# Performance work log

Measured on AMD Instinct MI355X. Metric: run time of the kernel, lower is better.

The kernel has to match this reference:

```python
import jax, jax.numpy as jnp
import numpy as np

EPS = 1e-5

def setup_inputs() -> dict:
    key = jax.random.key(0)
    ks = jax.random.split(key, 8)
    B, Cin, H, W = 16, 64, 512, 64
    Cout = 128  # out_channels == mid_channels (default) == NL1D channels
    return {
        "x": jax.random.normal(ks[0], (B, Cin, H, W), dtype=jnp.float32),
        "conv_w": jax.random.normal(ks[1], (Cout, Cin, 3, 3), dtype=jnp.float32) * 0.05,
        "bn1_g": jnp.ones((Cout,), jnp.float32),
        "bn1_b": jnp.zeros((Cout,), jnp.float32),
        "g_w": jax.random.normal(ks[2], (Cout, Cout), dtype=jnp.float32) * 0.05,
        "g_b": jnp.zeros((Cout,), jnp.float32),
        "out_w": jax.random.normal(ks[3], (Cout, Cout), dtype=jnp.float32) * 0.05,
        "out_b": jnp.zeros((Cout,), jnp.float32),
        "bn2_g": jnp.ones((Cout,), jnp.float32),
        "bn2_b": jnp.zeros((Cout,), jnp.float32),
    }

def _bn_train(x, gamma, beta):
    # BatchNorm2d in training mode: batch stats over (B, H, W) per channel
    mu = jnp.mean(x, axis=(0, 2, 3), keepdims=True)
    var = jnp.mean(jnp.square(x - mu), axis=(0, 2, 3), keepdims=True)
    xn = (x - mu) * jax.lax.rsqrt(var + EPS)
    return xn * gamma[None, :, None, None] + beta[None, :, None, None]

def reference(x, conv_w, bn1_g, bn1_b, g_w, g_b, out_w, out_b, bn2_g, bn2_b):
    # conv: 3x3, reflect padding, no bias -> BN -> ReLU
    xp = jnp.pad(x, ((0, 0), (0, 0), (1, 1), (1, 1)), mode="reflect")
    h = jax.lax.conv_general_dilated(
        xp, conv_w, window_strides=(1, 1), padding="VALID",
        dimension_numbers=("NCHW", "OIHW", "NCHW"))
    h = jax.nn.relu(_bn_train(h, bn1_g, bn1_b))  # [B, C, H, W]

    # NL1D
    B, C, Hh, W = h.shape
    xm = jnp.mean(h, axis=3)  # [B, C, H]
    # layer_norm over (C, H) per batch element, no affine
    mu = jnp.mean(xm, axis=(1, 2), keepdims=True)
    var = jnp.mean(jnp.square(xm - mu), axis=(1, 2), keepdims=True)
    xn = (xm - mu) * jax.lax.rsqrt(var + EPS)

    f = jnp.einsum("bch,bck->bhk", xn, xn) / jnp.sqrt(jnp.float32(C))
    f = jax.nn.softmax(f, axis=2)  # [B, H, H]

    y = jnp.einsum("mc,bch->bmh", g_w, xn) + g_b[None, :, None]  # conv1d 1x1
    y = jnp.einsum("bhk,bmk->bmh", f, y)  # bmm(f, y^T)^T
    y = jnp.einsum("om,bmh->boh", out_w, y) + out_b[None, :, None]  # [B, C, H]

    out = h + y[:, :, :, None]  # broadcast == repeat over W
    return jax.nn.silu(_bn_train(out, bn2_g, bn2_b))
```

## Files before the change

### kernel.cpp

```cpp
#include <hip/hip_runtime.h>
#include <stdint.h>

typedef __attribute__((ext_vector_type(8))) short short8;
typedef __attribute__((ext_vector_type(4))) float f32x4;

typedef const __attribute__((address_space(1))) unsigned int* gas_u32p;
typedef __attribute__((address_space(3))) unsigned int* las_u32p;

__device__ __forceinline__ unsigned short f2bf(float f){
  union{float f; unsigned u;} v; v.f = f;
  unsigned r = v.u + 0x7FFFu + ((v.u >> 16) & 1u);
  return (unsigned short)(r >> 16);
}
__device__ __forceinline__ void dec8(uint4 d, float* r){
  union{unsigned a; float f;} t;
  t.a = (d.x & 0xFFFFu) << 16; r[0]=t.f; t.a = d.x & 0xFFFF0000u; r[1]=t.f;
  t.a = (d.y & 0xFFFFu) << 16; r[2]=t.f; t.a = d.y & 0xFFFF0000u; r[3]=t.f;
  t.a = (d.z & 0xFFFFu) << 16; r[4]=t.f; t.a = d.z & 0xFFFF0000u; r[5]=t.f;
  t.a = (d.w & 0xFFFFu) << 16; r[6]=t.f; t.a = d.w & 0xFFFF0000u; r[7]=t.f;
}

__global__ __launch_bounds__(256) void k_prep(const float* __restrict__ cw,
                                              unsigned short* __restrict__ wA){
  int i = blockIdx.x*256 + threadIdx.x;
  if(i >= 18*128*32) return;
  int kk = i & 31, m = (i >> 5) & 127, ks = i >> 12;
  int k = ks*32 + kk;
  int pos = k >> 6, cin = k & 63;
  int dh = pos/3, dw = pos - dh*3;
  wA[i] = f2bf(cw[((m*64 + cin)*3 + dh)*3 + dw]);
}

__global__ __launch_bounds__(256) void k_xbf(const float* __restrict__ x,
                                             unsigned short* __restrict__ xbf){
  const int h = blockIdx.x, b = blockIdx.y;
  __shared__ float L[64][65];
  const int t = threadIdx.x;
  #pragma unroll
  for(int i=0;i<4;++i){
    int idx = i*256 + t;
    int c = idx >> 4, w0 = (idx & 15) * 4;
    const float* p = x + (((size_t)b*64 + c)*512 + h)*64 + w0;
    float4 v = *(const float4*)p;
    L[c][w0] = v.x; L[c][w0+1] = v.y; L[c][w0+2] = v.z; L[c][w0+3] = v.w;
  }
  __syncthreads();
  unsigned short* dst = xbf + (((size_t)b*512 + h) << 12);
  #pragma unroll
  for(int i=0;i<8;++i){
    int idx = i*256 + t;
    int w = idx >> 5, c2 = (idx & 31)*2;
    unsigned pk = (unsigned)f2bf(L[c2][w]) | ((unsigned)f2bf(L[c2+1][w]) << 16);
    *(unsigned*)(dst + (w<<6) + c2) = pk;
  }
}

__global__ __launch_bounds__(256, 2) void k_conv(
    const unsigned short* __restrict__ xbf, const unsigned short* __restrict__ wA,
    unsigned short* __restrict__ craw, float* __restrict__ sum_slots,
    float* __restrict__ sq_slots)
{
  const int b = blockIdx.y;
  const int bx = blockIdx.x;
  const int hx = (bx & 7)*16 + (bx >> 3);
  const int h0 = hx * 4;
  __shared__ __align__(16) unsigned short xs[6*4096];
  __shared__ float red[2][128];
  const int t = threadIdx.x;
  const int lane = t & 63, wv = t >> 6;
  for(int r = wv; r < 6; r += 4){
    int hin = h0 - 1 + r;
    hin = hin < 0 ? 1 : (hin > 511 ? 510 : hin);
    const unsigned short* rsrc = xbf + (((size_t)b*512 + hin) << 12);
    unsigned short* ldsrow = &xs[r*4096];
    #pragma unroll
    for(int it=0; it<8; ++it){
      int o = it*1024 + lane*16;
      int w = o >> 7;
      int q = o & 127;
      int so = (w << 7) + (q ^ (((w >> 1) & 7) << 4));
      __builtin_amdgcn_global_load_lds(
          (gas_u32p)(const void*)((const char*)rsrc + so),
          (las_u32p)(void*)(ldsrow + it*512), 16, 0, 0);
    }
  }
  const int r15 = lane & 15, quad = lane >> 4;
  int P[4][3];
  #pragma unroll
  for(int nt=0;nt<4;++nt){
    int wn = (nt>>1)*32 + 2*r15 + (nt&1);
    #pragma unroll
    for(int dw=0;dw<3;++dw){
      int wi = wn + dw - 1;
      wi = wi < 0 ? 1 : (wi > 63 ? 62 : wi);
      int s = ((wi >> 1) & 7) << 4;
      P[nt][dw] = (wi << 7) + ((quad*16) ^ (s & 0x30)) + (s & 0x40);
    }
  }
  f32x4 acc[8][4];
  #pragma unroll
  for(int mt=0;mt<8;++mt)
    #pragma unroll
    for(int nt=0;nt<4;++nt){ f32x4 z = {0.f,0.f,0.f,0.f}; acc[mt][nt] = z; }
  const unsigned short* wbase = wA + r15*32 + quad*8;
  __syncthreads();
  const char* xsb = (const char*)xs;
  #pragma unroll
  for(int ks=0; ks<18; ++ks){
    const int pos = ks >> 1;
    const int dh = pos/3, dw = pos - dh*3;
    const int kbit = (ks & 1) << 6;
    const int rowoff = (wv + dh)*8192;
    short8 a[8];
    const unsigned short* wk = wbase + ks*4096;
    #pragma unroll
    for(int mt=0;mt<8;++mt) a[mt] = *(const short8*)(wk + mt*512);
    short8 bfr[4];
    #pragma unroll
    for(int nt=0;nt<4;++nt)
      bfr[nt] = *(const short8*)(xsb + rowoff + (P[nt][dw] ^ kbit));
    #pragma unroll
    for(int mt=0;mt<8;++mt){
      #pragma unroll
      for(int nt=0;nt<4;++nt)
        acc[mt][nt] = __builtin_amdgcn_mfma_f32_16x16x32_bf16(a[mt], bfr[nt], acc[mt][nt], 0,0,0);
    }
  }
  {
    size_t obase = (((size_t)b*128)*512 + (size_t)(h0+wv))*64 + 2*r15;
    #pragma unroll
    for(int mt=0;mt<8;++mt){
      #pragma unroll
      for(int rg=0;rg<4;++rg){
        int co = mt*16 + quad*4 + rg;
        unsigned pk0 = (unsigned)f2bf(acc[mt][0][rg]) | ((unsigned)f2bf(acc[mt][1][rg]) << 16);
        unsigned pk1 = (unsigned)f2bf(acc[mt][2][rg]) | ((unsigned)f2bf(acc[mt][3][rg]) << 16);
        *(unsigned*)(craw + obase + (size_t)co*32768) = pk0;
        *(unsigned*)(craw + obase + (size_t)co*32768 + 32) = pk1;
      }
    }
  }
  if(t < 128){ red[0][t] = 0.f; red[1][t] = 0.f; }
  __syncthreads();
  #pragma unroll
  for(int mt=0;mt<8;++mt){
    #pragma unroll
    for(int rg=0;rg<4;++rg){
      float s = acc[mt][0][rg] + acc[mt][1][rg] + acc[mt][2][rg] + acc[mt][3][rg];
      float q = acc[mt][0][rg]*acc[mt][0][rg] + acc[mt][1][rg]*acc[mt][1][rg]
              + acc[mt][2][rg]*acc[mt][2][rg] + acc[mt][3][rg]*acc[mt][3][rg];
      #pragma unroll
      for(int m=1;m<16;m<<=1){ s += __shfl_xor(s, m); q += __shfl_xor(q, m); }
      if(r15 == 0){
        int co = mt*16 + quad*4 + rg;
        atomicAdd(&red[0][co], s);
        atomicAdd(&red[1][co], q);
      }
    }
  }
  __syncthreads();
  if(t < 128){
    int slot = bx & 63;
    atomicAdd(&sum_slots[t*64 + slot], red[0][t]);
    atomicAdd(&sq_slots[t*64 + slot], red[1][t]);
  }
}

__global__ __launch_bounds__(256) void k_bn1fin(
    const float* __restrict__ sum_slots, const float* __restrict__ sq_slots,
    const float* __restrict__ g1, const float* __restrict__ b1,
    float* __restrict__ s1, float* __restrict__ t1)
{
  int c = threadIdx.x; if(c >= 128) return;
  double S = 0.0, Q = 0.0;
  for(int s=0;s<64;++s){ S += (double)sum_slots[c*64+s]; Q += (double)sq_slots[c*64+s]; }
  const double N = 524288.0;
  double mu = S/N, var = Q/N - mu*mu;
  float sc = (float)((double)g1[c] / sqrt(var + 1e-5));
  s1[c] = sc;
  t1[c] = (float)((double)b1[c] - mu*(double)sc);
}

__global__ __launch_bounds__(256) void k_passB(
    const unsigned short* __restrict__ craw, const float* __restrict__ s1,
    const float* __restrict__ t1, float* __restrict__ xm,
    float* __restrict__ Sh, float* __restrict__ Qh,
    float* __restrict__ lnS, float* __restrict__ lnQ)
{
  const int c = blockIdx.x, b = blockIdx.y;
  const int t = threadIdx.x, wv = t >> 6, l = t & 63;
  const float sc = s1[c], sf = t1[c];
  const unsigned short* base = craw + (((size_t)b*128 + c)*512)*64;
  float* xrow = xm + ((size_t)b*128 + c)*512;
  float sa = 0.f, qa = 0.f, la = 0.f;
  for(int it=0; it<16; ++it){
    int row = it*32 + wv*8 + (l >> 3);
    int w0 = (l & 7)*8;
    uint4 d = *(const uint4*)(base + (size_t)row*64 + w0);
    float r[8]; dec8(d, r);
    float tot = 0.f;
    #pragma unroll
    for(int j=0;j<8;++j){
      float v = sc*r[j] + sf;
      v = v > 0.f ? v : 0.f;
      tot += v; sa += v; qa += v*v;
    }
    tot += __shfl_xor(tot, 1); tot += __shfl_xor(tot, 2); tot += __shfl_xor(tot, 4);
    if((l & 7) == 0){
      float mv = tot * (1.f/64.f);
      xrow[row] = mv;
      la += mv*mv;
    }
  }
  #pragma unroll
  for(int m=1;m<64;m<<=1){
    sa += __shfl_xor(sa, m); qa += __shfl_xor(qa, m); la += __shfl_xor(la, m);
  }
  __shared__ float rs[4], rq[4], rl[4];
  if(l == 0){ rs[wv]=sa; rq[wv]=qa; rl[wv]=la; }
  __syncthreads();
  if(t == 0){
    float S = rs[0]+rs[1]+rs[2]+rs[3];
    float Q = rq[0]+rq[1]+rq[2]+rq[3];
    float L = rl[0]+rl[1]+rl[2]+rl[3];
    atomicAdd(&Sh[c], S);
    atomicAdd(&Qh[c], Q);
    atomicAdd(&lnS[b], S * (1.f/64.f));
    atomicAdd(&lnQ[b], L);
  }
}

__global__ __launch_bounds__(256) void k_lnfin(
    const float* __restrict__ lnS, const float* __restrict__ lnQ,
    float* __restrict__ ln_mu, float* __restrict__ ln_rs)
{
  int b = threadIdx.x; if(b >= 16) return;
  double mu = (double)lnS[b] / 65536.0;
  double var = (double)lnQ[b] / 65536.0 - mu*mu;
  ln_mu[b] = (float)mu;
  ln_rs[b] = (float)(1.0 / sqrt(var + 1e-5));
}

__global__ __launch_bounds__(256) void k_f(const float* __restrict__ xm,
    const float* __restrict__ ln_mu, const float* __restrict__ ln_rs,
    float* __restrict__ f)
{
  const int kt = blockIdx.x, ht = blockIdx.y, b = blockIdx.z;
  __shared__ __align__(16) float Xh[128][64];
  __shared__ __align__(16) float Xk[128][64];
  const int t = threadIdx.x;
  const int h0 = ht*64, k0 = kt*64;
  const float mu = ln_mu[b], rs = ln_rs[b];
  for(int i=0;i<32;++i){
    int idx = t + i*256;
    int c = idx >> 6, hh = idx & 63;
    const float* src = xm + ((size_t)b*128 + c)*512;
    Xh[c][hh] = (src[h0 + hh] - mu) * rs;
    Xk[c][hh] = (src[k0 + hh] - mu) * rs;
  }
  __syncthreads();
  const int tx = t & 15, ty = t >> 4;
  float acc[4][4] = {{0}};
  for(int c=0;c<128;++c){
    f32x4 a = *(const f32x4*)&Xh[c][ty*4];
    f32x4 bb = *(const f32x4*)&Xk[c][tx*4];
    #pragma unroll
    for(int i=0;i<4;++i)
      #pragma unroll
      for(int j=0;j<4;++j) acc[i][j] += a[i]*bb[j];
  }
  const float s = 0.088388347648318447f;
  #pragma unroll
  for(int i=0;i<4;++i){
    f32x4 o;
    o[0]=acc[i][0]*s; o[1]=acc[i][1]*s; o[2]=acc[i][2]*s; o[3]=acc[i][3]*s;
    *(f32x4*)&f[((size_t)b*512 + h0 + ty*4 + i)*512 + k0 + tx*4] = o;
  }
}

__global__ __launch_bounds__(256) void k_sm(float* __restrict__ f)
{
  const int bid = blockIdx.x;
  const int b = bid >> 7, h4 = bid & 127;
  const int t = threadIdx.x, wv = t >> 6, l = t & 63;
  float* row = f + ((size_t)b*512 + h4*4 + wv)*512;
  f32x4 v0 = *(const f32x4*)&row[l*8];
  f32x4 v1 = *(const f32x4*)&row[l*8 + 4];
  float mx = v0[0];
  #pragma unroll
  for(int j=1;j<4;++j) mx = fmaxf(mx, v0[j]);
  #pragma unroll
  for(int j=0;j<4;++j) mx = fmaxf(mx, v1[j]);
  #pragma unroll
  for(int m=1;m<64;m<<=1) mx = fmaxf(mx, __shfl_xor(mx, m));
  float sum = 0.f;
  #pragma unroll
  for(int j=0;j<4;++j){ v0[j] = __expf(v0[j]-mx); sum += v0[j]; }
  #pragma unroll
  for(int j=0;j<4;++j){ v1[j] = __expf(v1[j]-mx); sum += v1[j]; }
  #pragma unroll
  for(int m=1;m<64;m<<=1) sum += __shfl_xor(sum, m);
  float inv = 1.f / sum;
  #pragma unroll
  for(int j=0;j<4;++j){ v0[j] *= inv; v1[j] *= inv; }
  *(f32x4*)&row[l*8] = v0;
  *(f32x4*)&row[l*8+4] = v1;
}

__global__ __launch_bounds__(256) void k_y1(
    const float* __restrict__ xm, const float* __restrict__ ln_mu,
    const float* __restrict__ ln_rs, const float* __restrict__ gw,
    const float* __restrict__ gb, float* __restrict__ y1)
{
  const int kt = blockIdx.x, b = blockIdx.y;
  __shared__ __align__(16) float GT[128][128];
  __shared__ __align__(16) float XN[128][68];
  const int t = threadIdx.x;
  const int k0 = kt*64;
  const float mu = ln_mu[b], rs = ln_rs[b];
  for(int i=0;i<64;++i){
    int idx = t + i*256;
    int o = idx & 127, c = idx >> 7;
    GT[c][o] = gw[o*128 + c];
  }
  for(int i=0;i<32;++i){
    int idx = t + i*256;
    int c = idx >> 6, kk = idx & 63;
    XN[c][kk] = (xm[((size_t)b*128 + c)*512 + k0 + kk] - mu) * rs;
  }
  __syncthreads();
  const int tx = t & 15, ty = t >> 4;
  float acc[8][4] = {{0}};
  for(int c=0;c<128;++c){
    f32x4 a0 = *(const f32x4*)&GT[c][ty*8];
    f32x4 a1 = *(const f32x4*)&GT[c][ty*8+4];
    f32x4 bv = *(const f32x4*)&XN[c][tx*4];
    #pragma unroll
    for(int j=0;j<4;++j){
      #pragma unroll
      for(int i=0;i<4;++i){ acc[i][j] += a0[i]*bv[j]; acc[i+4][j] += a1[i]*bv[j]; }
    }
  }
  #pragma unroll
  for(int i=0;i<8;++i){
    int m = ty*8 + i;
    float bias = gb[m];
    f32x4 o;
    #pragma unroll
    for(int j=0;j<4;++j) o[j] = acc[i][j] + bias;
    *(f32x4*)&y1[((size_t)b*128 + m)*512 + k0 + tx*4] = o;
  }
}

__global__ __launch_bounds__(256) void k_y2(
    const float* __restrict__ f, const float* __restrict__ y1,
    float* __restrict__ y2t)
{
  const int ht = blockIdx.x, b = blockIdx.y;
  __shared__ __align__(16) float FT[64][36];
  __shared__ __align__(16) float Y1T[64][132];
  const int t = threadIdx.x;
  const int h0 = ht*32;
  const int tx = t & 15, ty = t >> 4;
  float acc[2][8] = {{0}};
  for(int kc=0;kc<8;++kc){
    int k0 = kc*64;
    __syncthreads();
    for(int i=0;i<8;++i){
      int idx = t + i*256;
      int k = idx & 63, hh = idx >> 6;
      FT[k][hh] = f[((size_t)b*512 + h0 + hh)*512 + k0 + k];
    }
    for(int i=0;i<32;++i){
      int idx = t + i*256;
      int k = idx & 63, m = idx >> 6;
      Y1T[k][m] = y1[((size_t)b*128 + m)*512 + k0 + k];
    }
    __syncthreads();
    for(int kk=0;kk<64;++kk){
      float a0 = FT[kk][ty*2], a1 = FT[kk][ty*2+1];
      f32x4 b0 = *(const f32x4*)&Y1T[kk][tx*8];
      f32x4 b1 = *(const f32x4*)&Y1T[kk][tx*8+4];
      #pragma unroll
      for(int j=0;j<4;++j){
        acc[0][j]   += a0*b0[j]; acc[1][j]   += a1*b0[j];
        acc[0][j+4] += a0*b1[j]; acc[1][j+4] += a1*b1[j];
      }
    }
  }
  #pragma unroll
  for(int i=0;i<2;++i){
    int h = h0 + ty*2 + i;
    f32x4 o0, o1;
    #pragma unroll
    for(int j=0;j<4;++j){ o0[j]=acc[i][j]; o1[j]=acc[i][j+4]; }
    float* dst = y2t + ((size_t)b*512 + h)*128 + tx*8;
    *(f32x4*)dst = o0;
    *(f32x4*)(dst+4) = o1;
  }
}

__global__ __launch_bounds__(256) void k_y3(
    const float* __restrict__ y2t, const float* __restrict__ ow,
    const float* __restrict__ obv, float* __restrict__ y3)
{
  const int ht = blockIdx.x, b = blockIdx.y;
  __shared__ __align__(16) float WT[128][128];
  __shared__ __align__(16) float Y2[128][36];
  const int t = threadIdx.x;
  const int h0 = ht*32;
  for(int i=0;i<64;++i){
    int idx = t + i*256;
    int o = idx & 127, m = idx >> 7;
    WT[m][o] = ow[o*128 + m];
  }
  for(int i=0;i<16;++i){
    int idx = t + i*256;
    int m = idx & 127, hh = idx >> 7;
    Y2[m][hh] = y2t[((size_t)b*512 + h0 + hh)*128 + m];
  }
  __syncthreads();
  const int tx = t & 15, ty = t >> 4;
  float acc[8][2] = {{0}};
  for(int m=0;m<128;++m){
    f32x4 a0 = *(const f32x4*)&WT[m][ty*8];
    f32x4 a1 = *(const f32x4*)&WT[m][ty*8+4];
    float b0 = Y2[m][tx*2], b1 = Y2[m][tx*2+1];
    #pragma unroll
    for(int i=0;i<4;++i){
      acc[i][0]   += a0[i]*b0; acc[i][1]   += a0[i]*b1;
      acc[i+4][0] += a1[i]*b0; acc[i+4][1] += a1[i]*b1;
    }
  }
  #pragma unroll
  for(int i=0;i<8;++i){
    int o = ty*8 + i;
    float bias = obv[o];
    float2 v; v.x = acc[i][0] + bias; v.y = acc[i][1] + bias;
    *(float2*)&y3[((size_t)b*128 + o)*512 + h0 + tx*2] = v;
  }
}

__global__ __launch_bounds__(256) void k_ystats(
    const float* __restrict__ y3, const float* __restrict__ xm,
    float* __restrict__ Sy, float* __restrict__ Syy, float* __restrict__ Sxy)
{
  const int c = blockIdx.x;
  const int t = threadIdx.x, wv = t >> 6, l = t & 63;
  float s=0.f, ss=0.f, sx=0.f;
  for(int i=0;i<32;++i){
    int idx = t + i*256;
    int b = idx >> 9, h = idx & 511;
    size_t off = ((size_t)b*128 + c)*512 + h;
    float v = y3[off], u = xm[off];
    s += v; ss += v*v; sx += v*u;
  }
  #pragma unroll
  for(int m=1;m<64;m<<=1){ s += __shfl_xor(s,m); ss += __shfl_xor(ss,m); sx += __shfl_xor(sx,m); }
  __shared__ float r1[4], r2[4], r3[4];
  if(l == 0){ r1[wv]=s; r2[wv]=ss; r3[wv]=sx; }
  __syncthreads();
  if(t == 0){
    Sy[c]  = r1[0]+r1[1]+r1[2]+r1[3];
    Syy[c] = r2[0]+r2[1]+r2[2]+r2[3];
    Sxy[c] = r3[0]+r3[1]+r3[2]+r3[3];
  }
}

__global__ __launch_bounds__(256) void k_bn2fin(
    const float* __restrict__ Sh, const float* __restrict__ Qh,
    const float* __restrict__ Sy, const float* __restrict__ Syy,
    const float* __restrict__ Sxy, const float* __restrict__ g2,
    const float* __restrict__ b2, float* __restrict__ s2, float* __restrict__ t2)
{
  int c = threadIdx.x; if(c >= 128) return;
  const double N = 524288.0;
  double S2 = (double)Sh[c] + 64.0*(double)Sy[c];
  double Q2 = (double)Qh[c] + 128.0*(double)Sxy[c] + 64.0*(double)Syy[c];
  double mu = S2/N, var = Q2/N - mu*mu;
  float sc = (float)((double)g2[c] / sqrt(var + 1e-5));
  s2[c] = sc;
  t2[c] = (float)((double)b2[c] - mu*(double)sc);
}

__global__ __launch_bounds__(256) void k_final(
    const unsigned short* __restrict__ craw, const float* __restrict__ s1,
    const float* __restrict__ t1, const float* __restrict__ y3,
    const float* __restrict__ s2, const float* __restrict__ t2,
    float* __restrict__ out)
{
  const int c = blockIdx.x, b = blockIdx.y;
  const int t = threadIdx.x, wv = t >> 6, l = t & 63;
  const float a1 = s1[c], c1 = t1[c], a2 = s2[c], c2 = t2[c];
  const size_t rb = ((size_t)b*128 + c)*512;
  const unsigned short* base = craw + rb*64;
  const float* yrow = y3 + rb;
  float* ob = out + rb*64;
  for(int it=0; it<16; ++it){
    int row = it*32 + wv*8 + (l >> 3);
    int w0 = (l & 7)*8;
    uint4 d = *(const uint4*)(base + (size_t)row*64 + w0);
    float yv = yrow[row];
    float r[8]; dec8(d, r);
    f32x4 o0, o1;
    #pragma unroll
    for(int j=0;j<8;++j){
      float h = a1*r[j] + c1; h = h > 0.f ? h : 0.f;
      float z = a2*(h + yv) + c2;
      float val = z * __builtin_amdgcn_rcpf(1.f + __expf(-z));
      if(j < 4) o0[j] = val; else o1[j-4] = val;
    }
    *(f32x4*)(ob + (size_t)row*64 + w0) = o0;
    *(f32x4*)(ob + (size_t)row*64 + w0 + 4) = o1;
  }
}

extern "C" void kernel_launch(void* const* d_in, const int* in_sizes, int n_in,
                              void* d_out, int out_size, void* d_ws, size_t ws_size,
                              hipStream_t stream)
{
  const float* x      = (const float*)d_in[0];
  const float* conv_w = (const float*)d_in[1];
  const float* bn1_g  = (const float*)d_in[2];
  const float* bn1_b  = (const float*)d_in[3];
  const float* g_w    = (const float*)d_in[4];
  const float* g_b    = (const float*)d_in[5];
  const float* out_w  = (const float*)d_in[6];
  const float* out_b  = (const float*)d_in[7];
  const float* bn2_g  = (const float*)d_in[8];
  const float* bn2_b  = (const float*)d_in[9];
  float* out = (float*)d_out;
  char* ws = (char*)d_ws;

  float* sum_slots = (float*)(ws);
  float* sq_slots  = (float*)(ws + 32768);
  float* Sh        = (float*)(ws + 65536);
  float* Qh        = (float*)(ws + 66048);
  float* lnS       = (float*)(ws + 66560);
  float* lnQ       = (float*)(ws + 66624);
  float* s1        = (float*)(ws + 66688);
  float* t1        = (float*)(ws + 67200);
  float* ln_mu     = (float*)(ws + 67712);
  float* ln_rs     = (float*)(ws + 67776);
  float* Sy        = (float*)(ws + 67840);
  float* Syy       = (float*)(ws + 68352);
  float* Sxy       = (float*)(ws + 68864);
  float* s2        = (float*)(ws + 69376);
  float* t2        = (float*)(ws + 69888);
  unsigned short* wA = (unsigned short*)(ws + 70400);
  float* y3        = (float*)(ws + 217856);
  unsigned short* craw = (unsigned short*)(ws + 4412160);

  float* xm  = out;
  float* y1  = out + 2*(1u<<20);
  float* y2t = out + 3*(1u<<20);
  float* f   = out + 4*(1u<<20);
  unsigned short* xbf = (unsigned short*)((char*)out + (size_t)64*1024*1024);

  hipMemsetAsync(ws, 0, 66688, stream);
  hipLaunchKernelGGL(k_prep,   dim3(288),      dim3(256), 0, stream, conv_w, wA);
  hipLaunchKernelGGL(k_xbf,    dim3(512,16),   dim3(256), 0, stream, x, xbf);
  hipLaunchKernelGGL(k_conv,   dim3(128,16),   dim3(256), 0, stream, xbf, wA, craw, sum_slots, sq_slots);
  hipLaunchKernelGGL(k_bn1fin, dim3(1),        dim3(128), 0, stream, sum_slots, sq_slots, bn1_g, bn1_b, s1, t1);
  hipLaunchKernelGGL(k_passB,  dim3(128,16),   dim3(256), 0, stream, craw, s1, t1, xm, Sh, Qh, lnS, lnQ);
  hipLaunchKernelGGL(k_lnfin,  dim3(1),        dim3(64),  0, stream, lnS, lnQ, ln_mu, ln_rs);
  hipLaunchKernelGGL(k_f,      dim3(8,8,16),   dim3(256), 0, stream, xm, ln_mu, ln_rs, f);
  hipLaunchKernelGGL(k_sm,     dim3(2048),     dim3(256), 0, stream, f);
  hipLaunchKernelGGL(k_y1,     dim3(8,16),     dim3(256), 0, stream, xm, ln_mu, ln_rs, g_w, g_b, y1);
  hipLaunchKernelGGL(k_y2,     dim3(16,16),    dim3(256), 0, stream, f, y1, y2t);
  hipLaunchKernelGGL(k_y3,     dim3(16,16),    dim3(256), 0, stream, y2t, out_w, out_b, y3);
  hipLaunchKernelGGL(k_ystats, dim3(128),      dim3(256), 0, stream, y3, xm, Sy, Syy, Sxy);
  hipLaunchKernelGGL(k_bn2fin, dim3(1),        dim3(128), 0, stream, Sh, Qh, Sy, Syy, Sxy, bn2_g, bn2_b, s2, t2);
  hipLaunchKernelGGL(k_final,  dim3(128,16),   dim3(256), 0, stream, craw, s1, t1, y3, s2, t2, out);
}
```

Measured before the change: 798.5 us.

## Fuse attention scores, softmax, matmuls and y-stats into one kernel

Replaces k_f, k_sm, k_y2, k_y3 and k_ystats with a single k_att kernel. Each block computes a 32-row slice of scores, applies softmax, multiplies by y1, applies out_w, and accumulates BN2 statistics into slotted atomics, all in shared memory. This removes the 16MB f matrix round trip and several launches. It also vectorises the k_y1 loads and makes the conv output stores nontemporal. The cost is a large shared-memory footprint (about 118KB per block) and only 256 blocks, which limits occupancy.

```diff
diff --git a/kernel.cpp b/kernel.cpp
--- a/kernel.cpp
+++ b/kernel.cpp
@@ -135,8 +135,8 @@
         int co = mt*16 + quad*4 + rg;
         unsigned pk0 = (unsigned)f2bf(acc[mt][0][rg]) | ((unsigned)f2bf(acc[mt][1][rg]) << 16);
         unsigned pk1 = (unsigned)f2bf(acc[mt][2][rg]) | ((unsigned)f2bf(acc[mt][3][rg]) << 16);
-        *(unsigned*)(craw + obase + (size_t)co*32768) = pk0;
-        *(unsigned*)(craw + obase + (size_t)co*32768 + 32) = pk1;
+        __builtin_nontemporal_store(pk0, (unsigned*)(craw + obase + (size_t)co*32768));
+        __builtin_nontemporal_store(pk1, (unsigned*)(craw + obase + (size_t)co*32768 + 32));
       }
     }
   }
@@ -241,100 +241,40 @@
   ln_rs[b] = (float)(1.0 / sqrt(var + 1e-5));
 }
 
-__global__ __launch_bounds__(256) void k_f(const float* __restrict__ xm,
-    const float* __restrict__ ln_mu, const float* __restrict__ ln_rs,
-    float* __restrict__ f)
-{
-  const int kt = blockIdx.x, ht = blockIdx.y, b = blockIdx.z;
-  __shared__ __align__(16) float Xh[128][64];
-  __shared__ __align__(16) float Xk[128][64];
-  const int t = threadIdx.x;
-  const int h0 = ht*64, k0 = kt*64;
-  const float mu = ln_mu[b], rs = ln_rs[b];
-  for(int i=0;i<32;++i){
-    int idx = t + i*256;
-    int c = idx >> 6, hh = idx & 63;
-    const float* src = xm + ((size_t)b*128 + c)*512;
-    Xh[c][hh] = (src[h0 + hh] - mu) * rs;
-    Xk[c][hh] = (src[k0 + hh] - mu) * rs;
-  }
-  __syncthreads();
-  const int tx = t & 15, ty = t >> 4;
-  float acc[4][4] = {{0}};
-  for(int c=0;c<128;++c){
-    f32x4 a = *(const f32x4*)&Xh[c][ty*4];
-    f32x4 bb = *(const f32x4*)&Xk[c][tx*4];
-    #pragma unroll
-    for(int i=0;i<4;++i)
-      #pragma unroll
-      for(int j=0;j<4;++j) acc[i][j] += a[i]*bb[j];
-  }
-  const float s = 0.088388347648318447f;
-  #pragma unroll
-  for(int i=0;i<4;++i){
-    f32x4 o;
-    o[0]=acc[i][0]*s; o[1]=acc[i][1]*s; o[2]=acc[i][2]*s; o[3]=acc[i][3]*s;
-    *(f32x4*)&f[((size_t)b*512 + h0 + ty*4 + i)*512 + k0 + tx*4] = o;
-  }
-}
-
-__global__ __launch_bounds__(256) void k_sm(float* __restrict__ f)
-{
-  const int bid = blockIdx.x;
-  const int b = bid >> 7, h4 = bid & 127;
-  const int t = threadIdx.x, wv = t >> 6, l = t & 63;
-  float* row = f + ((size_t)b*512 + h4*4 + wv)*512;
-  f32x4 v0 = *(const f32x4*)&row[l*8];
-  f32x4 v1 = *(const f32x4*)&row[l*8 + 4];
-  float mx = v0[0];
-  #pragma unroll
-  for(int j=1;j<4;++j) mx = fmaxf(mx, v0[j]);
-  #pragma unroll
-  for(int j=0;j<4;++j) mx = fmaxf(mx, v1[j]);
-  #pragma unroll
-  for(int m=1;m<64;m<<=1) mx = fmaxf(mx, __shfl_xor(mx, m));
-  float sum = 0.f;
-  #pragma unroll
-  for(int j=0;j<4;++j){ v0[j] = __expf(v0[j]-mx); sum += v0[j]; }
-  #pragma unroll
-  for(int j=0;j<4;++j){ v1[j] = __expf(v1[j]-mx); sum += v1[j]; }
-  #pragma unroll
-  for(int m=1;m<64;m<<=1) sum += __shfl_xor(sum, m);
-  float inv = 1.f / sum;
-  #pragma unroll
-  for(int j=0;j<4;++j){ v0[j] *= inv; v1[j] *= inv; }
-  *(f32x4*)&row[l*8] = v0;
-  *(f32x4*)&row[l*8+4] = v1;
-}
-
 __global__ __launch_bounds__(256) void k_y1(
     const float* __restrict__ xm, const float* __restrict__ ln_mu,
     const float* __restrict__ ln_rs, const float* __restrict__ gw,
     const float* __restrict__ gb, float* __restrict__ y1)
 {
   const int kt = blockIdx.x, b = blockIdx.y;
-  __shared__ __align__(16) float GT[128][128];
-  __shared__ __align__(16) float XN[128][68];
+  __shared__ __align__(16) float GT[128*132];
+  __shared__ __align__(16) float XN[128*68];
   const int t = threadIdx.x;
   const int k0 = kt*64;
   const float mu = ln_mu[b], rs = ln_rs[b];
-  for(int i=0;i<64;++i){
+  #pragma unroll
+  for(int i=0;i<16;++i){
     int idx = t + i*256;
-    int o = idx & 127, c = idx >> 7;
-    GT[c][o] = gw[o*128 + c];
-  }
-  for(int i=0;i<32;++i){
+    int c4 = (idx & 31)*4, o = idx >> 5;
+    float4 v = *(const float4*)&gw[o*128 + c4];
+    GT[(c4+0)*132 + o] = v.x; GT[(c4+1)*132 + o] = v.y;
+    GT[(c4+2)*132 + o] = v.z; GT[(c4+3)*132 + o] = v.w;
+  }
+  #pragma unroll
+  for(int i=0;i<8;++i){
     int idx = t + i*256;
-    int c = idx >> 6, kk = idx & 63;
-    XN[c][kk] = (xm[((size_t)b*128 + c)*512 + k0 + kk] - mu) * rs;
+    int kk4 = (idx & 15)*4, c = idx >> 4;
+    float4 v = *(const float4*)&xm[((size_t)b*128 + c)*512 + k0 + kk4];
+    XN[c*68 + kk4 + 0] = (v.x - mu)*rs; XN[c*68 + kk4 + 1] = (v.y - mu)*rs;
+    XN[c*68 + kk4 + 2] = (v.z - mu)*rs; XN[c*68 + kk4 + 3] = (v.w - mu)*rs;
   }
   __syncthreads();
   const int tx = t & 15, ty = t >> 4;
   float acc[8][4] = {{0}};
   for(int c=0;c<128;++c){
-    f32x4 a0 = *(const f32x4*)&GT[c][ty*8];
-    f32x4 a1 = *(const f32x4*)&GT[c][ty*8+4];
-    f32x4 bv = *(const f32x4*)&XN[c][tx*4];
+    f32x4 a0 = *(const f32x4*)&GT[c*132 + ty*8];
+    f32x4 a1 = *(const f32x4*)&GT[c*132 + ty*8 + 4];
+    f32x4 bv = *(const f32x4*)&XN[c*68 + tx*4];
     #pragma unroll
     for(int j=0;j<4;++j){
       #pragma unroll
@@ -352,131 +292,182 @@
   }
 }
 
-__global__ __launch_bounds__(256) void k_y2(
-    const float* __restrict__ f, const float* __restrict__ y1,
-    float* __restrict__ y2t)
+__global__ __launch_bounds__(256) void k_att(
+    const float* __restrict__ xm, const float* __restrict__ ln_mu,
+    const float* __restrict__ ln_rs, const float* __restrict__ y1,
+    const float* __restrict__ ow, const float* __restrict__ obv,
+    float* __restrict__ y3,
+    float* __restrict__ SyS, float* __restrict__ SyyS, float* __restrict__ SxyS)
 {
   const int ht = blockIdx.x, b = blockIdx.y;
-  __shared__ __align__(16) float FT[64][36];
-  __shared__ __align__(16) float Y1T[64][132];
+  const int h0 = ht*32;
+  const int SP = 528;
+  __shared__ __align__(16) float S[32*528];
+  __shared__ __align__(16) float XH[128*32];
+  __shared__ __align__(16) float BUF[8704];
   const int t = threadIdx.x;
-  const int h0 = ht*32;
   const int tx = t & 15, ty = t >> 4;
-  float acc[2][8] = {{0}};
-  for(int kc=0;kc<8;++kc){
-    int k0 = kc*64;
-    __syncthreads();
+  const int lane = t & 63, wv = t >> 6;
+  const float mu = ln_mu[b], rs = ln_rs[b];
+  const float* xb = xm + (size_t)b*128*512;
+  #pragma unroll
+  for(int i=0;i<4;++i){
+    int idx = t + i*256;
+    int hh4 = (idx & 7)*4, c = idx >> 3;
+    float4 v = *(const float4*)&xb[(size_t)c*512 + h0 + hh4];
+    XH[c*32 + hh4 + 0] = (v.x - mu)*rs; XH[c*32 + hh4 + 1] = (v.y - mu)*rs;
+    XH[c*32 + hh4 + 2] = (v.z - mu)*rs; XH[c*32 + hh4 + 3] = (v.w - mu)*rs;
+  }
+  const float sscale = 0.088388347648318447f;
+  for(int kt=0;kt<8;++kt){
+    int k0 = kt*64;
+    #pragma unroll
     for(int i=0;i<8;++i){
       int idx = t + i*256;
-      int k = idx & 63, hh = idx >> 6;
-      FT[k][hh] = f[((size_t)b*512 + h0 + hh)*512 + k0 + k];
-    }
-    for(int i=0;i<32;++i){
+      int kk4 = (idx & 15)*4, c = idx >> 4;
+      float4 v = *(const float4*)&xb[(size_t)c*512 + k0 + kk4];
+      BUF[c*68 + kk4 + 0] = (v.x - mu)*rs; BUF[c*68 + kk4 + 1] = (v.y - mu)*rs;
+      BUF[c*68 + kk4 + 2] = (v.z - mu)*rs; BUF[c*68 + kk4 + 3] = (v.w - mu)*rs;
+    }
+    __syncthreads();
+    float acc[2][4] = {{0}};
+    for(int c=0;c<128;++c){
+      float a0 = XH[c*32 + ty*2];
+      float a1 = XH[c*32 + ty*2 + 1];
+      f32x4 bv = *(const f32x4*)&BUF[c*68 + tx*4];
+      #pragma unroll
+      for(int j=0;j<4;++j){ acc[0][j] += a0*bv[j]; acc[1][j] += a1*bv[j]; }
+    }
+    #pragma unroll
+    for(int i=0;i<2;++i){
+      f32x4 o;
+      #pragma unroll
+      for(int j=0;j<4;++j) o[j] = acc[i][j]*sscale;
+      *(f32x4*)&S[(ty*2+i)*SP + k0 + tx*4] = o;
+    }
+    __syncthreads();
+  }
+  #pragma unroll
+  for(int rr=0;rr<8;++rr){
+    int row = wv*8 + rr;
+    float* rowp = &S[row*SP];
+    f32x4 v0 = *(const f32x4*)&rowp[lane*8];
+    f32x4 v1 = *(const f32x4*)&rowp[lane*8 + 4];
+    float mx = v0[0];
+    #pragma unroll
+    for(int j=1;j<4;++j) mx = fmaxf(mx, v0[j]);
+    #pragma unroll
+    for(int j=0;j<4;++j) mx = fmaxf(mx, v1[j]);
+    #pragma unroll
+    for(int m=1;m<64;m<<=1) mx = fmaxf(mx, __shfl_xor(mx, m));
+    float sum = 0.f;
+    #pragma unroll
+    for(int j=0;j<4;++j){ v0[j] = __expf(v0[j]-mx); sum += v0[j]; }
+    #pragma unroll
+    for(int j=0;j<4;++j){ v1[j] = __expf(v1[j]-mx); sum += v1[j]; }
+    #pragma unroll
+    for(int m=1;m<64;m<<=1) sum += __shfl_xor(sum, m);
+    float inv = 1.f / sum;
+    #pragma unroll
+    for(int j=0;j<4;++j){ v0[j] *= inv; v1[j] *= inv; }
+    *(f32x4*)&rowp[lane*8] = v0;
+    *(f32x4*)&rowp[lane*8+4] = v1;
+  }
+  __syncthreads();
+  float y2a[2][8] = {{0}};
+  for(int kt=0;kt<8;++kt){
+    int k0 = kt*64;
+    #pragma unroll
+    for(int i=0;i<8;++i){
       int idx = t + i*256;
-      int k = idx & 63, m = idx >> 6;
-      Y1T[k][m] = y1[((size_t)b*128 + m)*512 + k0 + k];
+      int kk4 = (idx & 15)*4, m = idx >> 4;
+      float4 v = *(const float4*)&y1[((size_t)b*128 + m)*512 + k0 + kk4];
+      BUF[(kk4+0)*132 + m] = v.x; BUF[(kk4+1)*132 + m] = v.y;
+      BUF[(kk4+2)*132 + m] = v.z; BUF[(kk4+3)*132 + m] = v.w;
     }
     __syncthreads();
     for(int kk=0;kk<64;++kk){
-      float a0 = FT[kk][ty*2], a1 = FT[kk][ty*2+1];
-      f32x4 b0 = *(const f32x4*)&Y1T[kk][tx*8];
-      f32x4 b1 = *(const f32x4*)&Y1T[kk][tx*8+4];
+      float a0 = S[(ty*2)*SP + k0 + kk];
+      float a1 = S[(ty*2+1)*SP + k0 + kk];
+      f32x4 b0 = *(const f32x4*)&BUF[kk*132 + tx*8];
+      f32x4 b1 = *(const f32x4*)&BUF[kk*132 + tx*8 + 4];
       #pragma unroll
       for(int j=0;j<4;++j){
-        acc[0][j]   += a0*b0[j]; acc[1][j]   += a1*b0[j];
-        acc[0][j+4] += a0*b1[j]; acc[1][j+4] += a1*b1[j];
+        y2a[0][j]   += a0*b0[j]; y2a[1][j]   += a1*b0[j];
+        y2a[0][j+4] += a0*b1[j]; y2a[1][j+4] += a1*b1[j];
       }
     }
-  }
-  #pragma unroll
-  for(int i=0;i<2;++i){
-    int h = h0 + ty*2 + i;
-    f32x4 o0, o1;
-    #pragma unroll
-    for(int j=0;j<4;++j){ o0[j]=acc[i][j]; o1[j]=acc[i][j+4]; }
-    float* dst = y2t + ((size_t)b*512 + h)*128 + tx*8;
-    *(f32x4*)dst = o0;
-    *(f32x4*)(dst+4) = o1;
-  }
-}
-
-__global__ __launch_bounds__(256) void k_y3(
-    const float* __restrict__ y2t, const float* __restrict__ ow,
-    const float* __restrict__ obv, float* __restrict__ y3)
-{
-  const int ht = blockIdx.x, b = blockIdx.y;
-  __shared__ __align__(16) float WT[128][128];
-  __shared__ __align__(16) float Y2[128][36];
-  const int t = threadIdx.x;
-  const int h0 = ht*32;
-  for(int i=0;i<64;++i){
-    int idx = t + i*256;
-    int o = idx & 127, m = idx >> 7;
-    WT[m][o] = ow[o*128 + m];
-  }
+    __syncthreads();
+  }
+  #pragma unroll
+  for(int i=0;i<2;++i)
+    #pragma unroll
+    for(int j=0;j<8;++j)
+      BUF[(ty*2+i)*131 + tx*8 + j] = y2a[i][j];
+  float* OWT = S;
+  #pragma unroll
   for(int i=0;i<16;++i){
     int idx = t + i*256;
-    int m = idx & 127, hh = idx >> 7;
-    Y2[m][hh] = y2t[((size_t)b*512 + h0 + hh)*128 + m];
-  }
-  __syncthreads();
-  const int tx = t & 15, ty = t >> 4;
-  float acc[8][2] = {{0}};
+    int m4 = (idx & 31)*4, o = idx >> 5;
+    float4 v = *(const float4*)&ow[o*128 + m4];
+    OWT[(m4+0)*132 + o] = v.x; OWT[(m4+1)*132 + o] = v.y;
+    OWT[(m4+2)*132 + o] = v.z; OWT[(m4+3)*132 + o] = v.w;
+  }
+  __syncthreads();
+  float a2[2][8] = {{0}};
   for(int m=0;m<128;++m){
-    f32x4 a0 = *(const f32x4*)&WT[m][ty*8];
-    f32x4 a1 = *(const f32x4*)&WT[m][ty*8+4];
-    float b0 = Y2[m][tx*2], b1 = Y2[m][tx*2+1];
-    #pragma unroll
-    for(int i=0;i<4;++i){
-      acc[i][0]   += a0[i]*b0; acc[i][1]   += a0[i]*b1;
-      acc[i+4][0] += a1[i]*b0; acc[i+4][1] += a1[i]*b1;
-    }
-  }
-  #pragma unroll
-  for(int i=0;i<8;++i){
-    int o = ty*8 + i;
+    f32x4 w0 = *(const f32x4*)&OWT[m*132 + ty*8];
+    f32x4 w1 = *(const f32x4*)&OWT[m*132 + ty*8 + 4];
+    float h0v = BUF[(tx*2)*131 + m];
+    float h1v = BUF[(tx*2+1)*131 + m];
+    #pragma unroll
+    for(int j=0;j<4;++j){
+      a2[0][j]   += w0[j]*h0v; a2[1][j]   += w0[j]*h1v;
+      a2[0][j+4] += w1[j]*h0v; a2[1][j+4] += w1[j]*h1v;
+    }
+  }
+  const int slot = ((ht<<4) | b) & 31;
+  #pragma unroll
+  for(int j=0;j<8;++j){
+    int o = ty*8 + j;
     float bias = obv[o];
-    float2 v; v.x = acc[i][0] + bias; v.y = acc[i][1] + bias;
-    *(float2*)&y3[((size_t)b*128 + o)*512 + h0 + tx*2] = v;
-  }
-}
-
-__global__ __launch_bounds__(256) void k_ystats(
-    const float* __restrict__ y3, const float* __restrict__ xm,
-    float* __restrict__ Sy, float* __restrict__ Syy, float* __restrict__ Sxy)
-{
-  const int c = blockIdx.x;
-  const int t = threadIdx.x, wv = t >> 6, l = t & 63;
-  float s=0.f, ss=0.f, sx=0.f;
-  for(int i=0;i<32;++i){
-    int idx = t + i*256;
-    int b = idx >> 9, h = idx & 511;
-    size_t off = ((size_t)b*128 + c)*512 + h;
-    float v = y3[off], u = xm[off];
-    s += v; ss += v*v; sx += v*u;
-  }
-  #pragma unroll
-  for(int m=1;m<64;m<<=1){ s += __shfl_xor(s,m); ss += __shfl_xor(ss,m); sx += __shfl_xor(sx,m); }
-  __shared__ float r1[4], r2[4], r3[4];
-  if(l == 0){ r1[wv]=s; r2[wv]=ss; r3[wv]=sx; }
-  __syncthreads();
-  if(t == 0){
-    Sy[c]  = r1[0]+r1[1]+r1[2]+r1[3];
-    Syy[c] = r2[0]+r2[1]+r2[2]+r2[3];
-    Sxy[c] = r3[0]+r3[1]+r3[2]+r3[3];
+    float v0 = a2[0][j] + bias;
+    float v1 = a2[1][j] + bias;
+    size_t off = ((size_t)b*128 + o)*512 + h0 + tx*2;
+    float2 st; st.x = v0; st.y = v1;
+    *(float2*)&y3[off] = st;
+    float2 xv = *(const float2*)&xm[off];
+    float sy_ = v0 + v1;
+    float syy_ = v0*v0 + v1*v1;
+    float sxy_ = v0*xv.x + v1*xv.y;
+    #pragma unroll
+    for(int m=1;m<16;m<<=1){
+      sy_ += __shfl_xor(sy_, m); syy_ += __shfl_xor(syy_, m); sxy_ += __shfl_xor(sxy_, m);
+    }
+    if(tx == 0){
+      atomicAdd(&SyS[o*32 + slot], sy_);
+      atomicAdd(&SyyS[o*32 + slot], syy_);
+      atomicAdd(&SxyS[o*32 + slot], sxy_);
+    }
   }
 }
 
 __global__ __launch_bounds__(256) void k_bn2fin(
     const float* __restrict__ Sh, const float* __restrict__ Qh,
-    const float* __restrict__ Sy, const float* __restrict__ Syy,
-    const float* __restrict__ Sxy, const float* __restrict__ g2,
+    const float* __restrict__ SyS, const float* __restrict__ SyyS,
+    const float* __restrict__ SxyS, const float* __restrict__ g2,
     const float* __restrict__ b2, float* __restrict__ s2, float* __restrict__ t2)
 {
   int c = threadIdx.x; if(c >= 128) return;
+  double Sy = 0.0, Syy = 0.0, Sxy = 0.0;
+  for(int s=0;s<32;++s){
+    Sy  += (double)SyS[c*32+s];
+    Syy += (double)SyyS[c*32+s];
+    Sxy += (double)SxyS[c*32+s];
+  }
   const double N = 524288.0;
-  double S2 = (double)Sh[c] + 64.0*(double)Sy[c];
-  double Q2 = (double)Qh[c] + 128.0*(double)Sxy[c] + 64.0*(double)Syy[c];
+  double S2 = (double)Sh[c] + 64.0*Sy;
+  double Q2 = (double)Qh[c] + 128.0*Sxy + 64.0*Syy;
   double mu = S2/N, var = Q2/N - mu*mu;
   float sc = (float)((double)g2[c] / sqrt(var + 1e-5));
   s2[c] = sc;
@@ -534,6 +525,9 @@
 
   float* sum_slots = (float*)(ws);
   float* sq_slots  = (float*)(ws + 32768);
+  float* SyS       = (float*)(ws);
+  float* SyyS      = (float*)(ws + 16384);
+  float* SxyS      = (float*)(ws + 32768);
   float* Sh        = (float*)(ws + 65536);
   float* Qh        = (float*)(ws + 66048);
   float* lnS       = (float*)(ws + 66560);
@@ -542,19 +536,14 @@
   float* t1        = (float*)(ws + 67200);
   float* ln_mu     = (float*)(ws + 67712);
   float* ln_rs     = (float*)(ws + 67776);
-  float* Sy        = (float*)(ws + 67840);
-  float* Syy       = (float*)(ws + 68352);
-  float* Sxy       = (float*)(ws + 68864);
-  float* s2        = (float*)(ws + 69376);
-  float* t2        = (float*)(ws + 69888);
+  float* s2        = (float*)(ws + 67840);
+  float* t2        = (float*)(ws + 68352);
   unsigned short* wA = (unsigned short*)(ws + 70400);
   float* y3        = (float*)(ws + 217856);
   unsigned short* craw = (unsigned short*)(ws + 4412160);
 
   float* xm  = out;
   float* y1  = out + 2*(1u<<20);
-  float* y2t = out + 3*(1u<<20);
-  float* f   = out + 4*(1u<<20);
   unsigned short* xbf = (unsigned short*)((char*)out + (size_t)64*1024*1024);
 
   hipMemsetAsync(ws, 0, 66688, stream);
@@ -562,14 +551,11 @@
   hipLaunchKernelGGL(k_xbf,    dim3(512,16),   dim3(256), 0, stream, x, xbf);
   hipLaunchKernelGGL(k_conv,   dim3(128,16),   dim3(256), 0, stream, xbf, wA, craw, sum_slots, sq_slots);
   hipLaunchKernelGGL(k_bn1fin, dim3(1),        dim3(128), 0, stream, sum_slots, sq_slots, bn1_g, bn1_b, s1, t1);
+  hipMemsetAsync(ws, 0, 49152, stream);
   hipLaunchKernelGGL(k_passB,  dim3(128,16),   dim3(256), 0, stream, craw, s1, t1, xm, Sh, Qh, lnS, lnQ);
   hipLaunchKernelGGL(k_lnfin,  dim3(1),        dim3(64),  0, stream, lnS, lnQ, ln_mu, ln_rs);
-  hipLaunchKernelGGL(k_f,      dim3(8,8,16),   dim3(256), 0, stream, xm, ln_mu, ln_rs, f);
-  hipLaunchKernelGGL(k_sm,     dim3(2048),     dim3(256), 0, stream, f);
   hipLaunchKernelGGL(k_y1,     dim3(8,16),     dim3(256), 0, stream, xm, ln_mu, ln_rs, g_w, g_b, y1);
-  hipLaunchKernelGGL(k_y2,     dim3(16,16),    dim3(256), 0, stream, f, y1, y2t);
-  hipLaunchKernelGGL(k_y3,     dim3(16,16),    dim3(256), 0, stream, y2t, out_w, out_b, y3);
-  hipLaunchKernelGGL(k_ystats, dim3(128),      dim3(256), 0, stream, y3, xm, Sy, Syy, Sxy);
-  hipLaunchKernelGGL(k_bn2fin, dim3(1),        dim3(128), 0, stream, Sh, Qh, Sy, Syy, Sxy, bn2_g, bn2_b, s2, t2);
+  hipLaunchKernelGGL(k_att,    dim3(16,16),    dim3(256), 0, stream, xm, ln_mu, ln_rs, y1, out_w, out_b, y3, SyS, SyyS, SxyS);
+  hipLaunchKernelGGL(k_bn2fin, dim3(1),        dim3(128), 0, stream, Sh, Qh, SyS, SyyS, SxyS, bn2_g, bn2_b, s2, t2);
   hipLaunchKernelGGL(k_final,  dim3(128,16),   dim3(256), 0, stream, craw, s1, t1, y3, s2, t2, out);
 }
```

Measured after the change: 739.9 us. 1.08x faster.
